# Kernel optimization log

Measured on AMD Instinct MI355X. Metric: run time of the kernel, lower is better.

## Reference

```python
import jax, jax.numpy as jnp
import numpy as np


def setup_inputs() -> dict:
    key = jax.random.key(0)
    k1, k2 = jax.random.split(key)
    B, C, H, W, S = 8, 128, 256, 256, 1024
    inp = jax.random.normal(k1, (B, C, H, W), dtype=jnp.float32)
    seg = jax.random.randint(k2, (B, H, W), 0, S, dtype=jnp.int32)
    return {"input": inp, "segLabels": seg, "num_segments": S}


def reference(input, segLabels, num_segments):
    # input: [B, C, H, W] float; segLabels: [B, H, W] int in [0, S)
    B, C, H, W = input.shape
    S = num_segments
    N = H * W
    # [B, N, C] pixel features
    feats = jnp.transpose(input.reshape(B, C, N), (0, 2, 1))
    # offset labels so each image's segments occupy a disjoint id range
    ids = (segLabels.reshape(B, N) + jnp.arange(B, dtype=segLabels.dtype)[:, None] * S).reshape(-1)
    flat = feats.reshape(B * N, C)
    sums = jax.ops.segment_sum(flat, ids, num_segments=B * S)          # [B*S, C]
    counts = jax.ops.segment_sum(jnp.ones((B * N,), dtype=input.dtype), ids, num_segments=B * S)  # [B*S]
    avg = sums / jnp.maximum(counts, 1.0)[:, None]
    return avg.reshape(B, S, C)
```

## Files before the change

kernel.cpp:

```cpp
#include <hip/hip_runtime.h>


#define BB 8
#define CC 128
#define NPIX 65536
#define SS 1024
#define TILE 4096
#define NTILES (NPIX / TILE)
#define THREADS 1024

#define POS_ELEMS (BB * NPIX)
#define OFF_ELEMS (BB * NTILES * SS)

__global__ __launch_bounds__(THREADS, 1) void sort_kernel(
    const int* __restrict__ seg, unsigned short* __restrict__ pos,
    unsigned short* __restrict__ tileoff) {
  __shared__ unsigned int hist[SS];
  const int b   = blockIdx.x / NTILES;
  const int t   = blockIdx.x % NTILES;
  const int tid = threadIdx.x;

  hist[tid] = 0u;
  __syncthreads();

  const int base = b * NPIX + t * TILE;
  const int4 lab = reinterpret_cast<const int4*>(seg + base)[tid];
  const unsigned int r0 = atomicAdd(&hist[lab.x], 1u);
  const unsigned int r1 = atomicAdd(&hist[lab.y], 1u);
  const unsigned int r2 = atomicAdd(&hist[lab.z], 1u);
  const unsigned int r3 = atomicAdd(&hist[lab.w], 1u);
  __syncthreads();

  const unsigned int cnt = hist[tid];
  for (int off = 1; off < SS; off <<= 1) {
    const unsigned int v = (tid >= off) ? hist[tid - off] : 0u;
    __syncthreads();
    hist[tid] += v;
    __syncthreads();
  }
  const unsigned int excl = hist[tid] - cnt;
  tileoff[(b * NTILES + t) * SS + tid] = (unsigned short)excl;
  __syncthreads();
  hist[tid] = excl;
  __syncthreads();

  ushort4 p4;
  p4.x = (unsigned short)(hist[lab.x] + r0);
  p4.y = (unsigned short)(hist[lab.y] + r1);
  p4.z = (unsigned short)(hist[lab.z] + r2);
  p4.w = (unsigned short)(hist[lab.w] + r3);
  reinterpret_cast<ushort4*>(pos + base)[tid] = p4;
}

__global__ __launch_bounds__(THREADS, 1) void aggr_kernel(
    const float* __restrict__ inp, const unsigned short* __restrict__ pos,
    const unsigned short* __restrict__ tileoff, float* __restrict__ out) {
  __shared__ float4 buf[TILE];
  __shared__ unsigned short offl[SS + 1];

  const int b   = blockIdx.x >> 5;
  const int c0  = (blockIdx.x & 31) << 2;
  const int tid = threadIdx.x;

  const float4* __restrict__ pl0 =
      reinterpret_cast<const float4*>(inp + ((size_t)b * CC + c0) * NPIX);
  const int Q = NPIX / 4;

  float a0 = 0.f, a1 = 0.f, a2 = 0.f, a3 = 0.f;
  int cnt = 0;

  for (int t = 0; t < NTILES; ++t) {
    const int pbase = t * (TILE / 4);
    const float4 v0 = pl0[pbase + tid];
    const float4 v1 = pl0[pbase + tid + Q];
    const float4 v2 = pl0[pbase + tid + 2 * Q];
    const float4 v3 = pl0[pbase + tid + 3 * Q];
    const ushort4 p4 =
        reinterpret_cast<const ushort4*>(pos + b * NPIX + t * TILE)[tid];
    const unsigned short off_s = tileoff[(b * NTILES + t) * SS + tid];

    __syncthreads();
    if (tid == 0) offl[SS] = (unsigned short)TILE;
    offl[tid] = off_s;
    buf[p4.x] = make_float4(v0.x, v1.x, v2.x, v3.x);
    buf[p4.y] = make_float4(v0.y, v1.y, v2.y, v3.y);
    buf[p4.z] = make_float4(v0.z, v1.z, v2.z, v3.z);
    buf[p4.w] = make_float4(v0.w, v1.w, v2.w, v3.w);
    __syncthreads();

    const int beg = offl[tid];
    const int end = offl[tid + 1];
    cnt += end - beg;
    for (int j = beg; j < end; ++j) {
      const float4 v = buf[j];
      a0 += v.x; a1 += v.y; a2 += v.z; a3 += v.w;
    }
  }

  const float inv = 1.0f / (float)max(cnt, 1);
  reinterpret_cast<float4*>(out + ((size_t)(b * SS + tid)) * CC + c0)[0] =
      make_float4(a0 * inv, a1 * inv, a2 * inv, a3 * inv);
}

__global__ __launch_bounds__(THREADS, 1) void seg_avg_kernel(
    const float* __restrict__ inp, const int* __restrict__ seg,
    float* __restrict__ out) {
  __shared__ float acc[SS * 5];
  const int b   = blockIdx.x >> 5;
  const int c0  = (blockIdx.x & 31) << 2;
  const int tid = threadIdx.x;
  for (int i = tid; i < SS * 5; i += THREADS) acc[i] = 0.0f;
  __syncthreads();
  const float4* __restrict__ p0 =
      reinterpret_cast<const float4*>(inp + ((size_t)b * CC + c0) * NPIX);
  const int4* __restrict__ lab = reinterpret_cast<const int4*>(seg + (size_t)b * NPIX);
  const int Q = NPIX / 4;
  int* iacc = reinterpret_cast<int*>(acc);
  for (int i = 0; i < NPIX / (4 * THREADS); ++i) {
    const int p = i * THREADS + tid;
    const int4 s4 = lab[p];
    const float4 v0 = p0[p], v1 = p0[p + Q], v2 = p0[p + 2 * Q], v3 = p0[p + 3 * Q];
    const int a0 = s4.x * 5, a1 = s4.y * 5, a2 = s4.z * 5, a3 = s4.w * 5;
    unsafeAtomicAdd(&acc[a0 + 0], v0.x); unsafeAtomicAdd(&acc[a0 + 1], v1.x);
    unsafeAtomicAdd(&acc[a0 + 2], v2.x); unsafeAtomicAdd(&acc[a0 + 3], v3.x);
    atomicAdd(&iacc[a0 + 4], 1);
    unsafeAtomicAdd(&acc[a1 + 0], v0.y); unsafeAtomicAdd(&acc[a1 + 1], v1.y);
    unsafeAtomicAdd(&acc[a1 + 2], v2.y); unsafeAtomicAdd(&acc[a1 + 3], v3.y);
    atomicAdd(&iacc[a1 + 4], 1);
    unsafeAtomicAdd(&acc[a2 + 0], v0.z); unsafeAtomicAdd(&acc[a2 + 1], v1.z);
    unsafeAtomicAdd(&acc[a2 + 2], v2.z); unsafeAtomicAdd(&acc[a2 + 3], v3.z);
    atomicAdd(&iacc[a2 + 4], 1);
    unsafeAtomicAdd(&acc[a3 + 0], v0.w); unsafeAtomicAdd(&acc[a3 + 1], v1.w);
    unsafeAtomicAdd(&acc[a3 + 2], v2.w); unsafeAtomicAdd(&acc[a3 + 3], v3.w);
    atomicAdd(&iacc[a3 + 4], 1);
  }
  __syncthreads();
  for (int i = tid; i < SS * 4; i += THREADS) {
    const int s = i >> 2, c = i & 3;
    const float cntf = (float)iacc[s * 5 + 4];
    out[((size_t)(b * SS + s)) * CC + c0 + c] = acc[s * 5 + c] / fmaxf(cntf, 1.0f);
  }
}

extern "C" void kernel_launch(void* const* d_in, const int* in_sizes, int n_in,
                              void* d_out, int out_size, void* d_ws, size_t ws_size,
                              hipStream_t stream) {
  const float* inp = (const float*)d_in[0];
  const int*   seg = (const int*)d_in[1];
  float*       out = (float*)d_out;

  const size_t need = (size_t)POS_ELEMS * 2 + (size_t)OFF_ELEMS * 2;
  if (ws_size >= need) {
    unsigned short* pos  = (unsigned short*)d_ws;
    unsigned short* toff = pos + POS_ELEMS;
    sort_kernel<<<BB * NTILES, THREADS, 0, stream>>>(seg, pos, toff);
    aggr_kernel<<<BB * (CC / 4), THREADS, 0, stream>>>(inp, pos, toff, out);
  } else {
    seg_avg_kernel<<<BB * (CC / 4), THREADS, 0, stream>>>(inp, seg, out);
  }
}
```

Measured before the change: 371.8 us.

## Prefetch next tile in aggregation loop and use wave-shuffle scan in sort

The aggregation kernel now loads the next tile's input, positions and offsets into registers while the current tile is scattered into shared memory and reduced, so global loads overlap LDS work. Its barriers become a custom barrier that waits only on LDS counters and not on the outstanding global loads. The sort kernel's log-step shared-memory prefix scan, with two barriers per step, is replaced by a wavefront shuffle scan plus a 16-entry cross-wave scan. This raises register pressure and relies on inline asm for barrier semantics.

```diff
diff --git a/kernel.cpp b/kernel.cpp
--- a/kernel.cpp
+++ b/kernel.cpp
@@ -12,10 +12,15 @@
 #define POS_ELEMS (BB * NPIX)
 #define OFF_ELEMS (BB * NTILES * SS)
 
+__device__ __forceinline__ void lds_barrier() {
+  asm volatile("s_waitcnt lgkmcnt(0)\n\ts_barrier" ::: "memory");
+}
+
 __global__ __launch_bounds__(THREADS, 1) void sort_kernel(
     const int* __restrict__ seg, unsigned short* __restrict__ pos,
     unsigned short* __restrict__ tileoff) {
   __shared__ unsigned int hist[SS];
+  __shared__ unsigned int wsum[16];
   const int b   = blockIdx.x / NTILES;
   const int t   = blockIdx.x % NTILES;
   const int tid = threadIdx.x;
@@ -32,15 +37,28 @@
   __syncthreads();
 
   const unsigned int cnt = hist[tid];
-  for (int off = 1; off < SS; off <<= 1) {
-    const unsigned int v = (tid >= off) ? hist[tid - off] : 0u;
-    __syncthreads();
-    hist[tid] += v;
-    __syncthreads();
+  unsigned int v = cnt;
+  #pragma unroll
+  for (int off = 1; off < 64; off <<= 1) {
+    const unsigned int u = __shfl_up(v, off);
+    if ((tid & 63) >= off) v += u;
   }
-  const unsigned int excl = hist[tid] - cnt;
+  const int w = tid >> 6;
+  if ((tid & 63) == 63) wsum[w] = v;
+  __syncthreads();
+  if (tid < 16) {
+    unsigned int x = wsum[tid];
+    #pragma unroll
+    for (int off = 1; off < 16; off <<= 1) {
+      const unsigned int u = __shfl_up(x, off);
+      if (tid >= off) x += u;
+    }
+    wsum[tid] = x;
+  }
+  __syncthreads();
+  const unsigned int woff = (w == 0) ? 0u : wsum[w - 1];
+  const unsigned int excl = woff + v - cnt;
   tileoff[(b * NTILES + t) * SS + tid] = (unsigned short)excl;
-  __syncthreads();
   hist[tid] = excl;
   __syncthreads();
 
@@ -56,7 +74,7 @@
     const float* __restrict__ inp, const unsigned short* __restrict__ pos,
     const unsigned short* __restrict__ tileoff, float* __restrict__ out) {
   __shared__ float4 buf[TILE];
-  __shared__ unsigned short offl[SS + 1];
+  __shared__ unsigned short offl[SS + 2];
 
   const int b   = blockIdx.x >> 5;
   const int c0  = (blockIdx.x & 31) << 2;
@@ -64,30 +82,35 @@
 
   const float4* __restrict__ pl0 =
       reinterpret_cast<const float4*>(inp + ((size_t)b * CC + c0) * NPIX);
+  const ushort4* __restrict__ pos4 =
+      reinterpret_cast<const ushort4*>(pos + (size_t)b * NPIX);
   const int Q = NPIX / 4;
 
   float a0 = 0.f, a1 = 0.f, a2 = 0.f, a3 = 0.f;
   int cnt = 0;
 
+  float4 cv0 = pl0[tid], cv1 = pl0[tid + Q];
+  float4 cv2 = pl0[tid + 2 * Q], cv3 = pl0[tid + 3 * Q];
+  ushort4 cp4 = pos4[tid];
+  unsigned short coff = tileoff[(b * NTILES + 0) * SS + tid];
+
   for (int t = 0; t < NTILES; ++t) {
-    const int pbase = t * (TILE / 4);
-    const float4 v0 = pl0[pbase + tid];
-    const float4 v1 = pl0[pbase + tid + Q];
-    const float4 v2 = pl0[pbase + tid + 2 * Q];
-    const float4 v3 = pl0[pbase + tid + 3 * Q];
-    const ushort4 p4 =
-        reinterpret_cast<const ushort4*>(pos + b * NPIX + t * TILE)[tid];
-    const unsigned short off_s = tileoff[(b * NTILES + t) * SS + tid];
+    lds_barrier();
+    if (tid == 0) offl[SS] = (unsigned short)TILE;
+    offl[tid] = coff;
+    buf[cp4.x] = make_float4(cv0.x, cv1.x, cv2.x, cv3.x);
+    buf[cp4.y] = make_float4(cv0.y, cv1.y, cv2.y, cv3.y);
+    buf[cp4.z] = make_float4(cv0.z, cv1.z, cv2.z, cv3.z);
+    buf[cp4.w] = make_float4(cv0.w, cv1.w, cv2.w, cv3.w);
 
-    __syncthreads();
-    if (tid == 0) offl[SS] = (unsigned short)TILE;
-    offl[tid] = off_s;
-    buf[p4.x] = make_float4(v0.x, v1.x, v2.x, v3.x);
-    buf[p4.y] = make_float4(v0.y, v1.y, v2.y, v3.y);
-    buf[p4.z] = make_float4(v0.z, v1.z, v2.z, v3.z);
-    buf[p4.w] = make_float4(v0.w, v1.w, v2.w, v3.w);
-    __syncthreads();
+    const int tn = (t + 1 < NTILES) ? t + 1 : t;
+    const int pn = tn * (TILE / 4) + tid;
+    const float4 nv0 = pl0[pn], nv1 = pl0[pn + Q];
+    const float4 nv2 = pl0[pn + 2 * Q], nv3 = pl0[pn + 3 * Q];
+    const ushort4 np4 = pos4[pn];
+    const unsigned short noff = tileoff[(b * NTILES + tn) * SS + tid];
 
+    lds_barrier();
     const int beg = offl[tid];
     const int end = offl[tid + 1];
     cnt += end - beg;
@@ -95,6 +118,8 @@
       const float4 v = buf[j];
       a0 += v.x; a1 += v.y; a2 += v.z; a3 += v.w;
     }
+
+    cv0 = nv0; cv1 = nv1; cv2 = nv2; cv3 = nv3; cp4 = np4; coff = noff;
   }
 
   const float inv = 1.0f / (float)max(cnt, 1);
```

New measurement: 371.7 us. No clear change (-0.0%).
